# Performance work log

Measured on AMD Instinct MI355X. Metric: run time of the kernel, lower is better.

The kernel has to match this reference:

```python
import jax, jax.numpy as jnp
import numpy as np

LOG_2PI = jnp.float32(1.8378770664093453)


def setup_inputs() -> dict:
    key = jax.random.key(0)
    k_x, k_loc, k_scale, k_edges = jax.random.split(key, 4)
    B, C, M, N = 1024, 16, 4096, 8192
    x = jax.random.normal(k_x, (B, C), dtype=jnp.float32)
    locs = jax.random.normal(k_loc, (C, M), dtype=jnp.float32)
    scales = jax.random.uniform(k_scale, (C, M), dtype=jnp.float32)
    edges = jax.random.randint(k_edges, (C, N), 0, M, dtype=jnp.int32)
    return {"x": x, "locs": locs, "scales": scales, "edges": edges}


def reference(x, locs, scales, edges):
    # x: [B, C] -- one column per (univariate) child input layer
    # locs/scales: [C, M] Gaussian params per child-layer node
    # edges: [C, N] int -- edges[c, n] = child node in layer c feeding product node n
    C = locs.shape[0]
    s = scales + jnp.float32(0.5)  # keep scales strictly positive
    z = (x[:, :, None] - locs[None, :, :]) / s[None, :, :]
    ll = -0.5 * z * z - jnp.log(s)[None, :, :] - 0.5 * LOG_2PI  # [B, C, M]
    # gather per child layer and sum over child layers (product of likelihoods)
    cidx = jnp.arange(C)[:, None]  # [C, 1]
    gathered = ll[:, cidx, edges]  # [B, C, N]
    return gathered.sum(axis=1)  # [B, N]
```

## Files before the change

### kernel.cpp

```cpp
#include <hip/hip_runtime.h>

constexpr int BB = 1024;
constexpr int CC = 16;
constexpr int MM = 4096;
constexpr int NN = 8192;

constexpr int BLOCK   = 256;
constexpr int B_CHUNK = 32;

#define LOG_2PI 1.8378770664093453f

__global__ __launch_bounds__(BLOCK) void gm_gather_kernel(
    const float* __restrict__ x,
    const float* __restrict__ locs,
    const float* __restrict__ scales,
    const int*   __restrict__ edges,
    float* __restrict__ out)
{
    const int n  = blockIdx.x * BLOCK + threadIdx.x;
    const int b0 = blockIdx.y * B_CHUNK;

    __shared__ float xs[B_CHUNK * CC];
    for (int i = threadIdx.x; i < B_CHUNK * CC; i += BLOCK) {
        xs[i] = x[b0 * CC + i];
    }
    __syncthreads();

    float loc_r[CC];
    float inv_r[CC];
    float K = -0.5f * LOG_2PI * (float)CC;
#pragma unroll
    for (int c = 0; c < CC; ++c) {
        const int   e  = edges[c * NN + n];
        const float lc = locs[c * MM + e];
        const float s  = scales[c * MM + e] + 0.5f;
        loc_r[c] = lc;
        inv_r[c] = 1.0f / s;
        K       -= __logf(s);
    }

    float* outp = out + (size_t)b0 * NN + n;
#pragma unroll 4
    for (int bb = 0; bb < B_CHUNK; ++bb) {
        float acc = K;
#pragma unroll
        for (int c = 0; c < CC; ++c) {
            const float d = (xs[bb * CC + c] - loc_r[c]) * inv_r[c];
            acc = fmaf(d * d, -0.5f, acc);
        }
        outp[(size_t)bb * NN] = acc;
    }
}

extern "C" void kernel_launch(void* const* d_in, const int* in_sizes, int n_in,
                              void* d_out, int out_size, void* d_ws, size_t ws_size,
                              hipStream_t stream) {
    const float* x      = (const float*)d_in[0];
    const float* locs   = (const float*)d_in[1];
    const float* scales = (const float*)d_in[2];
    const int*   edges  = (const int*)d_in[3];
    float* out = (float*)d_out;

    dim3 grid(NN / BLOCK, BB / B_CHUNK);
    gm_gather_kernel<<<grid, dim3(BLOCK), 0, stream>>>(x, locs, scales, edges, out);
}
```

Before: 95.48 us.

## Precompute gathered Gaussian coefficients per product node in a separate prologue kernel

Splits the work into two kernels. The first gathers locs/scales through edges once per product node and writes loc, reciprocal scale and the log-normaliser constant to workspace. The second streams over batch chunks and reads these coalesced coefficients. This removes the redundant random gathers and the log/reciprocal work that each of the 32 batch-chunk blocks per column used to repeat. In exchange it adds a second launch and a workspace round trip of about 1 MB.

Measured after the change: 89.26 us. 6.5% less time.

```diff
diff --git a/kernel.cpp b/kernel.cpp
--- a/kernel.cpp
+++ b/kernel.cpp
@@ -10,11 +10,37 @@
 
 #define LOG_2PI 1.8378770664093453f
 
-__global__ __launch_bounds__(BLOCK) void gm_gather_kernel(
-    const float* __restrict__ x,
+__global__ __launch_bounds__(BLOCK) void coeff_kernel(
     const float* __restrict__ locs,
     const float* __restrict__ scales,
     const int*   __restrict__ edges,
+    float* __restrict__ loc_w,
+    float* __restrict__ inv_w,
+    float* __restrict__ k_w)
+{
+    const int n = blockIdx.x * BLOCK + threadIdx.x;
+
+    int e[CC];
+#pragma unroll
+    for (int c = 0; c < CC; ++c) e[c] = edges[c * NN + n];
+
+    float K = -0.5f * LOG_2PI * (float)CC;
+#pragma unroll
+    for (int c = 0; c < CC; ++c) {
+        const float lc = locs[c * MM + e[c]];
+        const float s  = scales[c * MM + e[c]] + 0.5f;
+        loc_w[c * NN + n] = lc;
+        inv_w[c * NN + n] = 1.0f / s;
+        K -= __logf(s);
+    }
+    k_w[n] = K;
+}
+
+__global__ __launch_bounds__(BLOCK) void stream_kernel(
+    const float* __restrict__ x,
+    const float* __restrict__ loc_w,
+    const float* __restrict__ inv_w,
+    const float* __restrict__ k_w,
     float* __restrict__ out)
 {
     const int n  = blockIdx.x * BLOCK + threadIdx.x;
@@ -28,16 +54,12 @@
 
     float loc_r[CC];
     float inv_r[CC];
-    float K = -0.5f * LOG_2PI * (float)CC;
 #pragma unroll
     for (int c = 0; c < CC; ++c) {
-        const int   e  = edges[c * NN + n];
-        const float lc = locs[c * MM + e];
-        const float s  = scales[c * MM + e] + 0.5f;
-        loc_r[c] = lc;
-        inv_r[c] = 1.0f / s;
-        K       -= __logf(s);
+        loc_r[c] = loc_w[c * NN + n];
+        inv_r[c] = inv_w[c * NN + n];
     }
+    const float K = k_w[n];
 
     float* outp = out + (size_t)b0 * NN + n;
 #pragma unroll 4
@@ -61,6 +83,13 @@
     const int*   edges  = (const int*)d_in[3];
     float* out = (float*)d_out;
 
-    dim3 grid(NN / BLOCK, BB / B_CHUNK);
-    gm_gather_kernel<<<grid, dim3(BLOCK), 0, stream>>>(x, locs, scales, edges, out);
+    float* loc_w = (float*)d_ws;
+    float* inv_w = loc_w + (size_t)CC * NN;
+    float* k_w   = inv_w + (size_t)CC * NN;
+
+    coeff_kernel<<<dim3(NN / BLOCK), dim3(BLOCK), 0, stream>>>(
+        locs, scales, edges, loc_w, inv_w, k_w);
+
+    stream_kernel<<<dim3(NN / BLOCK, BB / B_CHUNK), dim3(BLOCK), 0, stream>>>(
+        x, loc_w, inv_w, k_w, out);
 }
```

## Precompute quadratic coefficients in a separate kernel and stream two outputs per thread

Applied to the files above, without the earlier changes.

Splits the work into a coefficient kernel and a streaming kernel. The coefficient kernel gathers the per-(n,c) Gaussian parameters once and expands the log-likelihood into a quadratic in x, writing (a, b) pairs plus a summed constant to workspace. The streaming kernel then evaluates two FMAs per child using precomputed x and x^2 in shared memory, handles two n per thread, and writes float2 stores. This removes the redundant gathers and divides that each batch-chunk block used to repeat, at the cost of an extra launch and a workspace round trip, with possible rounding differences from the expanded form.

After: 90.25 us. 1.06x faster.

```diff
diff --git a/kernel.cpp b/kernel.cpp
--- a/kernel.cpp
+++ b/kernel.cpp
@@ -5,50 +5,88 @@
 constexpr int MM = 4096;
 constexpr int NN = 8192;
 
-constexpr int BLOCK   = 256;
-constexpr int B_CHUNK = 32;
-
 #define LOG_2PI 1.8378770664093453f
 
-__global__ __launch_bounds__(BLOCK) void gm_gather_kernel(
-    const float* __restrict__ x,
+__global__ __launch_bounds__(256) void coeff_kernel(
     const float* __restrict__ locs,
     const float* __restrict__ scales,
     const int*   __restrict__ edges,
+    float2* __restrict__ coef2,
+    float*  __restrict__ k_w)
+{
+    const int tid = threadIdx.x;
+    const int m   = tid & 15;
+    const int c   = tid >> 4;
+    const int n   = blockIdx.x * 16 + m;
+
+    const int   e  = edges[c * NN + n];
+    const float lc = locs[c * MM + e];
+    const float s  = scales[c * MM + e] + 0.5f;
+    const float inv = 1.0f / s;
+    const float a   = -0.5f * inv * inv;
+
+    coef2[(size_t)n * 16 + c] = make_float2(a, -2.0f * a * lc);
+
+    __shared__ float lg[256];
+    lg[m * 16 + c] = fmaf(a, lc * lc, -__logf(s)) - 0.5f * LOG_2PI;
+    __syncthreads();
+    if (tid < 16) {
+        float K = 0.0f;
+#pragma unroll
+        for (int cc = 0; cc < 16; ++cc) K += lg[tid * 16 + cc];
+        k_w[blockIdx.x * 16 + tid] = K;
+    }
+}
+
+constexpr int BLOCK   = 256;
+constexpr int NPT     = 2;
+constexpr int B_CHUNK = 32;
+
+__global__ __launch_bounds__(BLOCK) void stream_kernel(
+    const float*  __restrict__ x,
+    const float2* __restrict__ coef2,
+    const float*  __restrict__ k_w,
     float* __restrict__ out)
 {
-    const int n  = blockIdx.x * BLOCK + threadIdx.x;
-    const int b0 = blockIdx.y * B_CHUNK;
+    const int tid = threadIdx.x;
+    const int n   = blockIdx.x * (BLOCK * NPT) + tid * NPT;
+    const int b0  = blockIdx.y * B_CHUNK;
 
     __shared__ float xs[B_CHUNK * CC];
-    for (int i = threadIdx.x; i < B_CHUNK * CC; i += BLOCK) {
-        xs[i] = x[b0 * CC + i];
+    __shared__ float xs2[B_CHUNK * CC];
+    for (int i = tid; i < B_CHUNK * CC; i += BLOCK) {
+        const float v = x[b0 * CC + i];
+        xs[i]  = v;
+        xs2[i] = v * v;
     }
     __syncthreads();
 
-    float loc_r[CC];
-    float inv_r[CC];
-    float K = -0.5f * LOG_2PI * (float)CC;
+    float p2a[CC], p1a[CC], p2b[CC], p1b[CC];
 #pragma unroll
     for (int c = 0; c < CC; ++c) {
-        const int   e  = edges[c * NN + n];
-        const float lc = locs[c * MM + e];
-        const float s  = scales[c * MM + e] + 0.5f;
-        loc_r[c] = lc;
-        inv_r[c] = 1.0f / s;
-        K       -= __logf(s);
+        const float2 qa = coef2[(size_t)n * 16 + c];
+        const float2 qb = coef2[(size_t)(n + 1) * 16 + c];
+        p2a[c] = qa.x; p1a[c] = qa.y;
+        p2b[c] = qb.x; p1b[c] = qb.y;
     }
+    const float Ka = k_w[n];
+    const float Kb = k_w[n + 1];
 
     float* outp = out + (size_t)b0 * NN + n;
-#pragma unroll 4
+#pragma unroll 2
     for (int bb = 0; bb < B_CHUNK; ++bb) {
-        float acc = K;
+        float a0 = Ka, a1 = 0.0f, b0a = Kb, b1 = 0.0f;
 #pragma unroll
-        for (int c = 0; c < CC; ++c) {
-            const float d = (xs[bb * CC + c] - loc_r[c]) * inv_r[c];
-            acc = fmaf(d * d, -0.5f, acc);
+        for (int c = 0; c < CC; c += 2) {
+            const float xv0 = xs[bb * CC + c],     x20 = xs2[bb * CC + c];
+            const float xv1 = xs[bb * CC + c + 1], x21 = xs2[bb * CC + c + 1];
+            a0  = fmaf(x20, p2a[c],     fmaf(xv0, p1a[c],     a0));
+            a1  = fmaf(x21, p2a[c + 1], fmaf(xv1, p1a[c + 1], a1));
+            b0a = fmaf(x20, p2b[c],     fmaf(xv0, p1b[c],     b0a));
+            b1  = fmaf(x21, p2b[c + 1], fmaf(xv1, p1b[c + 1], b1));
         }
-        outp[(size_t)bb * NN] = acc;
+        *reinterpret_cast<float2*>(outp + (size_t)bb * NN) =
+            make_float2(a0 + a1, b0a + b1);
     }
 }
 
@@ -61,6 +99,12 @@
     const int*   edges  = (const int*)d_in[3];
     float* out = (float*)d_out;
 
-    dim3 grid(NN / BLOCK, BB / B_CHUNK);
-    gm_gather_kernel<<<grid, dim3(BLOCK), 0, stream>>>(x, locs, scales, edges, out);
+    float2* coef2 = (float2*)d_ws;
+    float*  k_w   = (float*)d_ws + (size_t)2 * CC * NN;
+
+    coeff_kernel<<<dim3(NN / 16), dim3(256), 0, stream>>>(
+        locs, scales, edges, coef2, k_w);
+
+    stream_kernel<<<dim3(NN / (BLOCK * NPT), BB / B_CHUNK), dim3(BLOCK), 0, stream>>>(
+        x, coef2, k_w, out);
 }
```
